# Kernel optimization log

Measured on AMD Instinct MI355X. Metric: run time of the kernel, lower is better.

Reference implementation:

```python
import jax, jax.numpy as jnp
import numpy as np

H = 32          # num query heads
KV = 8          # num kv heads
D = 64          # head_dim
WIN = 512       # sliding_window
BASE = 10000.0  # rope base


def setup_inputs() -> dict:
    key = jax.random.key(0)
    ks = jax.random.split(key, 5)
    B, S, DIM = 2, 2048, 2048
    x = jax.random.normal(ks[0], (B, S, DIM), dtype=jnp.float32)
    wq = jax.random.normal(ks[1], (H * D, DIM), dtype=jnp.float32) * 0.02
    wk = jax.random.normal(ks[2], (KV * D, DIM), dtype=jnp.float32) * 0.02
    wv = jax.random.normal(ks[3], (KV * D, DIM), dtype=jnp.float32) * 0.02
    wo = jax.random.normal(ks[4], (DIM, H * D), dtype=jnp.float32) * 0.02
    return {"x": x, "wq": wq, "wk": wk, "wv": wv, "wo": wo}


def _rope_tables(S):
    inv_freq = 1.0 / (BASE ** (jnp.arange(0, D, 2, dtype=jnp.float32) / D))
    t = jnp.arange(S, dtype=jnp.float32)
    freqs = t[:, None] * inv_freq[None, :]          # [S, D/2]
    emb = jnp.concatenate([freqs, freqs], axis=-1)  # [S, D]
    return jnp.cos(emb)[:, None, :], jnp.sin(emb)[:, None, :]  # [S,1,D]


def _rotate_half(u):
    return jnp.concatenate([-u[..., D // 2:], u[..., :D // 2]], axis=-1)


def reference(x, wq, wk, wv, wo):
    B, S, _ = x.shape
    q = (x @ wq.T).reshape(B, S, H, D)
    k = (x @ wk.T).reshape(B, S, KV, D)
    v = (x @ wv.T).reshape(B, S, KV, D)

    cos, sin = _rope_tables(S)  # [S,1,D] broadcasts over batch and heads
    q = q * cos + _rotate_half(q) * sin
    k = k * cos + _rotate_half(k) * sin

    q = q.transpose(0, 2, 1, 3)                        # [B,H,S,D]
    k = jnp.repeat(k.transpose(0, 2, 1, 3), H // KV, axis=1)  # [B,H,S,D]
    v = jnp.repeat(v.transpose(0, 2, 1, 3), H // KV, axis=1)

    scale = 1.0 / jnp.sqrt(jnp.float32(D))
    scores = jnp.einsum('bhqd,bhkd->bhqk', q, k) * scale  # [B,H,S,S]

    i = jnp.arange(S)[:, None]
    j = jnp.arange(S)[None, :]
    window_mask = jnp.abs(i - j) > WIN // 2   # True = masked (outside window)
    causal_mask = j > i                        # True = masked (future)
    masked = window_mask | causal_mask
    scores = jnp.where(masked[None, None], -jnp.inf, scores)

    attn = jax.nn.softmax(scores, axis=-1)
    out = jnp.einsum('bhqk,bhkd->bhqd', attn, v)  # [B,H,S,D]
    out = out.transpose(0, 2, 1, 3).reshape(B, S, H * D)
    return out @ wo.T
```

## Files before the change

kernel.cpp:

```cpp
#include <hip/hip_runtime.h>
#include <cstdint>
#include <cstddef>

#define SLEN 2048
#define NB 2
#define NH 32
#define NKV 8
#define HD 64
#define MROWS 4096
#define QDIM 2048
#define KVDIM 512
#define WINH 256

typedef float f32x4 __attribute__((ext_vector_type(4)));
typedef __bf16 bf16x8 __attribute__((ext_vector_type(8)));

__device__ __forceinline__ unsigned short f2bf(float f) {
  union { float f; unsigned u; } v; v.f = f;
  unsigned r = v.u + 0x7fffu + ((v.u >> 16) & 1u);
  return (unsigned short)(r >> 16);
}
__device__ __forceinline__ float bf2f(unsigned short h) {
  union { unsigned u; float f; } v; v.u = ((unsigned)h) << 16;
  return v.f;
}
__device__ __forceinline__ unsigned pk2(float a, float b) {
  return (unsigned)f2bf(a) | ((unsigned)f2bf(b) << 16);
}
__device__ __forceinline__ unsigned cvtpk(float a, float b) {
  unsigned r;
  asm("v_cvt_pk_bf16_f32 %0, %1, %2" : "=v"(r) : "v"(a), "v"(b));
  return r;
}
__device__ __forceinline__ uint4 cvt16(float4 a, float4 b) {
  uint4 u;
  u.x = pk2(a.x, a.y); u.y = pk2(a.z, a.w);
  u.z = pk2(b.x, b.y); u.w = pk2(b.z, b.w);
  return u;
}
__device__ __forceinline__ void async16(const unsigned short* g, unsigned short* l) {
  __builtin_amdgcn_global_load_lds(
      (const __attribute__((address_space(1))) unsigned int*)g,
      (__attribute__((address_space(3))) unsigned int*)l, 16, 0, 0);
}

__global__ void conv_xw(const float* __restrict__ x,
                        const float* __restrict__ wq, const float* __restrict__ wk,
                        const float* __restrict__ wv,
                        unsigned short* __restrict__ xb, unsigned short* __restrict__ wqkvb,
                        float2* __restrict__ tab) {
  size_t t = (size_t)blockIdx.x * 256 + threadIdx.x;
  if (t < (size_t)1048576) {
    size_t e = t * 8;
    float4 a = *(const float4*)(x + e);
    float4 b = *(const float4*)(x + e + 4);
    *(uint4*)(xb + e) = cvt16(a, b);
  } else if (t < (size_t)1835008) {
    size_t e = (t - 1048576) * 8;
    int row = (int)(e >> 11);
    const float* src; size_t off;
    if (row < 2048)       { src = wq; off = e; }
    else if (row < 2560)  { src = wk; off = e - (size_t)2048 * 2048; }
    else                  { src = wv; off = e - (size_t)2560 * 2048; }
    float4 a = *(const float4*)(src + off);
    float4 b = *(const float4*)(src + off + 4);
    *(uint4*)(wqkvb + e) = cvt16(a, b);
  } else {
    int id = (int)(t - 1835008);
    int d = id & 31;
    int s = id >> 5;
    float inv = expf((float)d * (-2.0f / 64.0f) * 9.210340371976184f);
    float ang = (float)s * inv;
    float sn, cs;
    sincosf(ang, &sn, &cs);
    tab[id] = make_float2(cs, sn);
  }
}

__global__ void rope_qk(unsigned short* __restrict__ qb,
                        unsigned short* __restrict__ kb,
                        const float* __restrict__ tabf) {
  const float2* tab = (const float2*)tabf;
  int tid = blockIdx.x * 256 + threadIdx.x;
  int oct = tid & 3;
  int head = (tid >> 2) % 40;
  int row = tid / 160;
  int s = row & (SLEN - 1);
  int d0 = oct * 8;
  unsigned short* p = (head < NH)
      ? qb + (size_t)row * QDIM + head * HD
      : kb + (size_t)row * KVDIM + (head - NH) * HD;
  uint4 u0 = *(const uint4*)(p + d0);
  uint4 u1 = *(const uint4*)(p + d0 + 32);
  const unsigned short* a16 = (const unsigned short*)&u0;
  const unsigned short* b16 = (const unsigned short*)&u1;
  unsigned short o0[8], o1[8];
#pragma unroll
  for (int j = 0; j < 8; ++j) {
    float2 cs = tab[s * 32 + d0 + j];
    float a = bf2f(a16[j]), b = bf2f(b16[j]);
    o0[j] = f2bf(a * cs.x - b * cs.y);
    o1[j] = f2bf(b * cs.x + a * cs.y);
  }
  *(uint4*)(p + d0)      = *(const uint4*)o0;
  *(uint4*)(p + d0 + 32) = *(const uint4*)o1;
}

__global__ __launch_bounds__(512, 2) void qkv_gemm(
    const unsigned short* __restrict__ Ap, const unsigned short* __restrict__ Bp,
    unsigned short* __restrict__ o_q, unsigned short* __restrict__ o_k,
    unsigned short* __restrict__ o_v)
{
  extern __shared__ unsigned short L[];
  constexpr int NT = 32;

  const int bid = blockIdx.x;
  const int swz = (bid & 7) * 32 + (bid >> 3);
  const int bm0 = (swz & 15) * 256;
  const int bn0 = (swz >> 4) * 192;

  const int tid = threadIdx.x;
  const int lane = tid & 63, wid = tid >> 6;
  const int g = lane >> 4, cl = lane & 15;
  const int wm = wid >> 2, wn = wid & 3;

  const int r0 = wid * 32 + (lane >> 2);
  const int s0 = (((lane & 3) ^ ((lane >> 3) & 3)) << 3);
  const unsigned short* gA = Ap + (size_t)(bm0 + r0) * 2048 + s0;
  const unsigned short* gB = Bp + (size_t)(bn0 + r0) * 2048 + s0;

  const int slotus = ((g ^ ((cl >> 1) & 3)) << 3);
  const int aread = (wm * 128 + cl) * 32 + slotus;
  const int bread = (wn * 48 + cl) * 32 + slotus;

#define REG_(b, op, kh) ((((b) * 2 + (op)) * 2 + (kh)) * 8192)
#define STG(op, kh, tt, db) do { \
    const unsigned short* s_ = ((op) ? gB : gA) + (tt) * 64 + (kh) * 32; \
    unsigned short* d_ = L + REG_(db, op, kh) + wid * 1024; \
    async16(s_, d_); \
    async16(s_ + 16 * 2048, d_ + 512); \
  } while (0)
#define LDA(dst, kh, mh) \
    _Pragma("unroll") for (int mf = 0; mf < 4; ++mf) \
      dst[mf] = *(const bf16x8*)&L[REG_(cb, 0, kh) + aread + (mh) * 2048 + mf * 512];
#define LDB(dst, kh) \
    _Pragma("unroll") for (int nf = 0; nf < 3; ++nf) \
      dst[nf] = *(const bf16x8*)&L[REG_(cb, 1, kh) + bread + nf * 512];
#define MM(mh, A, B) do { \
    __builtin_amdgcn_s_setprio(1); \
    _Pragma("unroll") for (int mf = 0; mf < 4; ++mf) \
      _Pragma("unroll") for (int nf = 0; nf < 3; ++nf) \
        acc[(mh) * 4 + mf][nf] = __builtin_amdgcn_mfma_f32_16x16x32_bf16( \
            A[mf], B[nf], acc[(mh) * 4 + mf][nf], 0, 0, 0); \
    __builtin_amdgcn_s_setprio(0); \
  } while (0)

  f32x4 acc[8][3] = {};

  STG(0, 0, 0, 0); STG(1, 0, 0, 0); STG(0, 1, 0, 0); STG(1, 1, 0, 0);
  STG(0, 0, 1, 1); STG(1, 0, 1, 1);
  asm volatile("s_waitcnt vmcnt(4)" ::: "memory");
  __builtin_amdgcn_s_barrier();
  __builtin_amdgcn_sched_barrier(0);

#pragma unroll 1
  for (int t = 0; t < NT; ++t) {
    const int cb = t & 1, nb = cb ^ 1;
    bf16x8 a00[4], a10[4], a01[4], a11[4], b0[3], b1[3];

    if (t + 1 < NT) STG(0, 1, t + 1, nb);
    LDA(a00, 0, 0); LDB(b0, 0);
    if (t + 1 < NT) STG(1, 1, t + 1, nb);
    LDA(a10, 0, 1);
    MM(0, a00, b0);
    LDA(a01, 1, 0); LDB(b1, 1);
    MM(1, a10, b0);
    asm volatile("s_waitcnt lgkmcnt(0)" ::: "memory");
    __builtin_amdgcn_s_barrier();
    __builtin_amdgcn_sched_barrier(0);
    if (t + 2 < NT) STG(0, 0, t + 2, cb);
    LDA(a11, 1, 1);
    MM(0, a01, b1);
    if (t + 2 < NT) STG(1, 0, t + 2, cb);
    MM(1, a11, b1);
    if (t + 2 < NT) { asm volatile("s_waitcnt vmcnt(4)" ::: "memory"); }
    else            { asm volatile("s_waitcnt vmcnt(0)" ::: "memory"); }
    asm volatile("s_waitcnt lgkmcnt(0)" ::: "memory");
    __builtin_amdgcn_s_barrier();
    __builtin_amdgcn_sched_barrier(0);
  }
#undef MM
#undef LDB
#undef LDA
#undef STG
#undef REG_

  const int rb = bm0 + wm * 128;
#pragma unroll
  for (int m = 0; m < 8; ++m)
#pragma unroll
    for (int nf = 0; nf < 3; ++nf) {
      const int col = bn0 + wn * 48 + nf * 16 + cl;
      if (col < QDIM) {
#pragma unroll
        for (int p = 0; p < 4; ++p) {
          int row = rb + m * 16 + g * 4 + p;
          o_q[(size_t)row * QDIM + col] = f2bf(acc[m][nf][p]);
        }
      } else if (col < QDIM + KVDIM) {
#pragma unroll
        for (int p = 0; p < 4; ++p) {
          int row = rb + m * 16 + g * 4 + p;
          o_k[(size_t)row * KVDIM + col - QDIM] = f2bf(acc[m][nf][p]);
        }
      } else {
        int vc = col - QDIM - KVDIM;
        int kvh = vc >> 6, d = vc & 63;
        int row0 = rb + m * 16 + g * 4;
        int bb = row0 >> 11, s = row0 & (SLEN - 1);
        unsigned short* dst = o_v + (((size_t)(bb * NKV + kvh) * HD + d) << 11) + s;
        uint2 u;
        u.x = pk2(acc[m][nf][0], acc[m][nf][1]);
        u.y = pk2(acc[m][nf][2], acc[m][nf][3]);
        *(uint2*)dst = u;
      }
    }
}

__global__ __launch_bounds__(512, 2) void out_gemm(
    const unsigned short* __restrict__ Ap, const unsigned short* __restrict__ Bp,
    float* __restrict__ o_f)
{
  extern __shared__ unsigned short L[];
  constexpr int NT = 32;

  const int bid = blockIdx.x;
  const int swz = (bid & 7) * 32 + (bid >> 3);
  const int bm0 = (swz & 31) * 128;
  const int bn0 = (swz >> 5) * 256;

  const int tid = threadIdx.x;
  const int lane = tid & 63, wid = tid >> 6;
  const int g = lane >> 4, cl = lane & 15;
  const int wm = wid >> 2, wn = wid & 3;

  const int s0 = (((lane & 3) ^ ((lane >> 3) & 3)) << 3);
  const unsigned short* gA = Ap + (size_t)(bm0 + wid * 16 + (lane >> 2)) * 2048 + s0;
  const unsigned short* gB = Bp + (size_t)(bn0 + wid * 32 + (lane >> 2)) * 2048 + s0;

  const int slotus = ((g ^ ((cl >> 1) & 3)) << 3);
  const int aread = (wm * 64 + cl) * 32 + slotus;
  const int bread = (wn * 64 + cl) * 32 + slotus;

#define REGA_(b, kh) ((b) * 24576 + (kh) * 4096)
#define REGB_(b, kh) ((b) * 24576 + 8192 + (kh) * 8192)
#define STGA(kh, tt, db) \
    async16(gA + (tt) * 64 + (kh) * 32, L + REGA_(db, kh) + wid * 512)
#define STGB(kh, tt, db) do { \
    const unsigned short* s_ = gB + (tt) * 64 + (kh) * 32; \
    unsigned short* d_ = L + REGB_(db, kh) + wid * 1024; \
    async16(s_, d_); \
    async16(s_ + 16 * 2048, d_ + 512); \
  } while (0)
#define LA(dst, kh, mp) \
    _Pragma("unroll") for (int mf = 0; mf < 2; ++mf) \
      dst[mf] = *(const bf16x8*)&L[REGA_(cb, kh) + aread + (mp) * 1024 + mf * 512];
#define LB(dst, kh) \
    _Pragma("unroll") for (int nf = 0; nf < 4; ++nf) \
      dst[nf] = *(const bf16x8*)&L[REGB_(cb, kh) + bread + nf * 512];
#define MMO(mp, A, B) do { \
    __builtin_amdgcn_s_setprio(1); \
    _Pragma("unroll") for (int mf = 0; mf < 2; ++mf) \
      _Pragma("unroll") for (int nf = 0; nf < 4; ++nf) \
        acc[(mp) * 2 + mf][nf] = __builtin_amdgcn_mfma_f32_16x16x32_bf16( \
            A[mf], B[nf], acc[(mp) * 2 + mf][nf], 0, 0, 0); \
    __builtin_amdgcn_s_setprio(0); \
  } while (0)

  f32x4 acc[4][4] = {};

  STGA(0, 0, 0); STGB(0, 0, 0); STGA(1, 0, 0); STGB(1, 0, 0);
  STGA(0, 1, 1); STGB(0, 1, 1);
  asm volatile("s_waitcnt vmcnt(3)" ::: "memory");
  __builtin_amdgcn_s_barrier();
  __builtin_amdgcn_sched_barrier(0);

#pragma unroll 1
  for (int t = 0; t < NT; ++t) {
    const int cb = t & 1, nb = cb ^ 1;
    bf16x8 p00[2], p10[2], p01[2], p11[2], b0[4], b1[4];

    if (t + 1 < NT) STGA(1, t + 1, nb);
    LA(p00, 0, 0); LB(b0, 0);
    if (t + 1 < NT) STGB(1, t + 1, nb);
    LA(p10, 0, 1);
    MMO(0, p00, b0);
    LA(p01, 1, 0); LB(b1, 1);
    MMO(1, p10, b0);
    asm volatile("s_waitcnt lgkmcnt(0)" ::: "memory");
    __builtin_amdgcn_s_barrier();
    __builtin_amdgcn_sched_barrier(0);
    if (t + 2 < NT) STGA(0, t + 2, cb);
    LA(p11, 1, 1);
    MMO(0, p01, b1);
    if (t + 2 < NT) STGB(0, t + 2, cb);
    MMO(1, p11, b1);
    if (t + 2 < NT) { asm volatile("s_waitcnt vmcnt(3)" ::: "memory"); }
    else            { asm volatile("s_waitcnt vmcnt(0)" ::: "memory"); }
    asm volatile("s_waitcnt lgkmcnt(0)" ::: "memory");
    __builtin_amdgcn_s_barrier();
    __builtin_amdgcn_sched_barrier(0);
  }
#undef MMO
#undef LB
#undef LA
#undef STGB
#undef STGA
#undef REGB_
#undef REGA_

  const int rb = bm0 + wm * 64;
  const int colb = bn0 + wn * 64;
#pragma unroll
  for (int m = 0; m < 4; ++m)
#pragma unroll
    for (int nf = 0; nf < 4; ++nf)
#pragma unroll
      for (int p = 0; p < 4; ++p) {
        int row = rb + m * 16 + g * 4 + p;
        o_f[(size_t)row * 2048 + colb + nf * 16 + cl] = acc[m][nf][p];
      }
}

__global__ __launch_bounds__(256) void attn(
    const unsigned short* __restrict__ qb, const unsigned short* __restrict__ kb,
    const unsigned short* __restrict__ vt, unsigned short* __restrict__ ao,
    const float* __restrict__ wo, unsigned short* __restrict__ wob)
{
  if (blockIdx.x >= 1024) {
    size_t t = (size_t)(blockIdx.x - 1024) * 256 + threadIdx.x;
    size_t e = t * 8;
    float4 a = *(const float4*)(wo + e);
    float4 b = *(const float4*)(wo + e + 4);
    *(uint4*)(wob + e) = cvt16(a, b);
    return;
  }

  __shared__ __align__(16) unsigned short Plds[4][2][16][40];
  const int lane = threadIdx.x & 63, wid = threadIdx.x >> 6;
  const int g = lane >> 4, cl = lane & 15;
  const int qt = blockIdx.x * 4 + wid;
  const int bh = qt >> 6, tl = qt & 63;
  const int i0 = tl * 32;
  const int b = bh >> 5, h = bh & 31, kvh = (bh & 31) >> 2;
  const int qi0 = i0 + cl, qi1 = i0 + 16 + cl;

  const unsigned short* qp0 = qb + ((size_t)(b * SLEN + qi0) * NH + h) * HD + g * 8;
  const unsigned short* qp1 = qb + ((size_t)(b * SLEN + qi1) * NH + h) * HD + g * 8;
  bf16x8 qf00 = *(const bf16x8*)qp0, qf01 = *(const bf16x8*)(qp0 + 32);
  bf16x8 qf10 = *(const bf16x8*)qp1, qf11 = *(const bf16x8*)(qp1 + 32);

  const unsigned short* kbase = kb + ((size_t)b * SLEN * NKV + kvh) * HD + g * 8;
  const unsigned short* vbase = vt + ((size_t)(b * NKV + kvh) * HD) * SLEN;

  f32x4 acc0[4] = {}, acc1[4] = {};
  float m0 = -1e30f, l0 = 0.f, m1 = -1e30f, l1 = 0.f;
  const int jb = (i0 > WINH) ? (i0 - WINH) : 0;

#define LOADK(dst, jj) do { \
    _Pragma("unroll") for (int t = 0; t < 2; ++t) { \
      int krow = (jj) + 16 * t + cl; \
      if (krow > SLEN - 1) krow = SLEN - 1; \
      const unsigned short* kp_ = kbase + (size_t)krow * KVDIM; \
      dst[t * 2]     = *(const bf16x8*)kp_; \
      dst[t * 2 + 1] = *(const bf16x8*)(kp_ + 32); \
    } \
  } while (0)

#define LOADV(dst, jj) do { \
    int jv = (jj) + g * 8; \
    if (jv > SLEN - 8) jv = SLEN - 8; \
    _Pragma("unroll") for (int vb2 = 0; vb2 < 4; ++vb2) \
      dst[vb2] = *(const bf16x8*)(vbase + (size_t)(vb2 * 16 + cl) * SLEN + jv); \
  } while (0)

#define SOFTMAX(SAC, MR, LR, ACC, QI, QF) do { \
    float sm[2][4]; float mx = -1e30f; \
    _Pragma("unroll") for (int t = 0; t < 2; ++t) \
      _Pragma("unroll") for (int p = 0; p < 4; ++p) { \
        int kj = j0 + 16 * t + 4 * g + p; \
        bool ok = (kj <= (QI)) && ((QI) - kj <= WINH); \
        float v = ok ? SAC[t][p] * 0.125f : -1e30f; \
        sm[t][p] = v; mx = fmaxf(mx, v); \
      } \
    mx = fmaxf(mx, __shfl_xor(mx, 16)); \
    mx = fmaxf(mx, __shfl_xor(mx, 32)); \
    float mnew = fmaxf(MR, mx); \
    float corr = __expf(MR - mnew); \
    float ps = 0.f; unsigned pw00, pw01, pw10, pw11; \
    { \
      float p0 = __expf(sm[0][0] - mnew), p1 = __expf(sm[0][1] - mnew); \
      float p2 = __expf(sm[0][2] - mnew), p3 = __expf(sm[0][3] - mnew); \
      ps += p0 + p1 + p2 + p3; pw00 = cvtpk(p0, p1); pw01 = cvtpk(p2, p3); \
      float p4 = __expf(sm[1][0] - mnew), p5 = __expf(sm[1][1] - mnew); \
      float p6 = __expf(sm[1][2] - mnew), p7 = __expf(sm[1][3] - mnew); \
      ps += p4 + p5 + p6 + p7; pw10 = cvtpk(p4, p5); pw11 = cvtpk(p6, p7); \
    } \
    ps += __shfl_xor(ps, 16); ps += __shfl_xor(ps, 32); \
    LR = LR * corr + ps; MR = mnew; \
    _Pragma("unroll") for (int vb2 = 0; vb2 < 4; ++vb2) \
      _Pragma("unroll") for (int p = 0; p < 4; ++p) ACC[vb2][p] *= corr; \
    *(unsigned*)&Plds[wid][QF][cl][4 * g]          = pw00; \
    *(unsigned*)&Plds[wid][QF][cl][4 * g + 2]      = pw01; \
    *(unsigned*)&Plds[wid][QF][cl][16 + 4 * g]     = pw10; \
    *(unsigned*)&Plds[wid][QF][cl][16 + 4 * g + 2] = pw11; \
  } while (0)

#define BODY(KC, KN, VC, VN) do { \
    LOADK(KN, j0 + 32);                           \
    LOADV(VN, j0 + 32);                           \
    f32x4 s0[2], s1[2]; \
    _Pragma("unroll") for (int t = 0; t < 2; ++t) { \
      f32x4 z = {}; \
      z = __builtin_amdgcn_mfma_f32_16x16x32_bf16(KC[t * 2], qf00, z, 0, 0, 0); \
      z = __builtin_amdgcn_mfma_f32_16x16x32_bf16(KC[t * 2 + 1], qf01, z, 0, 0, 0); \
      s0[t] = z; \
      f32x4 z2 = {}; \
      z2 = __builtin_amdgcn_mfma_f32_16x16x32_bf16(KC[t * 2], qf10, z2, 0, 0, 0); \
      z2 = __builtin_amdgcn_mfma_f32_16x16x32_bf16(KC[t * 2 + 1], qf11, z2, 0, 0, 0); \
      s1[t] = z2; \
    } \
    SOFTMAX(s0, m0, l0, acc0, qi0, 0); \
    SOFTMAX(s1, m1, l1, acc1, qi1, 1); \
    bf16x8 pf0 = *(const bf16x8*)&Plds[wid][0][cl][g * 8]; \
    bf16x8 pf1 = *(const bf16x8*)&Plds[wid][1][cl][g * 8]; \
    _Pragma("unroll") for (int vb2 = 0; vb2 < 4; ++vb2) \
      acc0[vb2] = __builtin_amdgcn_mfma_f32_16x16x32_bf16(VC[vb2], pf0, acc0[vb2], 0, 0, 0); \
    _Pragma("unroll") for (int vb2 = 0; vb2 < 4; ++vb2) \
      acc1[vb2] = __builtin_amdgcn_mfma_f32_16x16x32_bf16(VC[vb2], pf1, acc1[vb2], 0, 0, 0); \
  } while (0)

  bf16x8 kA[4], kB[4], vA[4], vB[4];
  LOADK(kA, jb); LOADV(vA, jb);
  int j0 = jb;
  for (;;) {
    BODY(kA, kB, vA, vB); j0 += 32; if (j0 > i0) break;
    BODY(kB, kA, vB, vA); j0 += 32; if (j0 > i0) break;
  }
#undef BODY
#undef SOFTMAX
#undef LOADV
#undef LOADK

  float inv0 = 1.0f / l0, inv1 = 1.0f / l1;
  unsigned short* op0 = ao + ((size_t)(b * SLEN + qi0) * NH + h) * HD;
  unsigned short* op1 = ao + ((size_t)(b * SLEN + qi1) * NH + h) * HD;
#pragma unroll
  for (int vbk = 0; vbk < 4; ++vbk) {
    *(unsigned*)(op0 + vbk * 16 + g * 4)     = cvtpk(acc0[vbk][0] * inv0, acc0[vbk][1] * inv0);
    *(unsigned*)(op0 + vbk * 16 + g * 4 + 2) = cvtpk(acc0[vbk][2] * inv0, acc0[vbk][3] * inv0);
    *(unsigned*)(op1 + vbk * 16 + g * 4)     = cvtpk(acc1[vbk][0] * inv1, acc1[vbk][1] * inv1);
    *(unsigned*)(op1 + vbk * 16 + g * 4 + 2) = cvtpk(acc1[vbk][2] * inv1, acc1[vbk][3] * inv1);
  }
}

extern "C" void kernel_launch(void* const* d_in, const int* in_sizes, int n_in,
                              void* d_out, int out_size, void* d_ws, size_t ws_size,
                              hipStream_t stream) {
  const float* x  = (const float*)d_in[0];
  const float* wq = (const float*)d_in[1];
  const float* wk = (const float*)d_in[2];
  const float* wv = (const float*)d_in[3];
  const float* wo = (const float*)d_in[4];
  float* out = (float*)d_out;

  char* w = (char*)d_ws;
  unsigned short* wqkvb = (unsigned short*)w; w += (size_t)3136 * 2048 * 2;
  unsigned short* xb    = (unsigned short*)w; w += (size_t)MROWS * QDIM * 2;
  unsigned short* qb    = (unsigned short*)w; w += (size_t)MROWS * QDIM * 2;
  unsigned short* kb    = (unsigned short*)w; w += (size_t)MROWS * KVDIM * 2;
  unsigned short* vt    = (unsigned short*)w; w += (size_t)MROWS * KVDIM * 2;
  float* tab            = (float*)w;          w += (size_t)SLEN * 32 * 8;
  unsigned short* wob = wqkvb;
  unsigned short* ao  = xb;

  hipFuncSetAttribute((const void*)qkv_gemm,
                      hipFuncAttributeMaxDynamicSharedMemorySize, 131072);
  hipFuncSetAttribute((const void*)out_gemm,
                      hipFuncAttributeMaxDynamicSharedMemorySize, 98304);

  conv_xw<<<7424, 256, 0, stream>>>(x, wq, wk, wv, xb, wqkvb, (float2*)tab);
  qkv_gemm<<<256, 512, 131072, stream>>>(xb, wqkvb, qb, kb, vt);
  rope_qk<<<(MROWS * 40 * 4) / 256, 256, 0, stream>>>(qb, kb, tab);
  attn<<<3072, 256, 0, stream>>>(qb, kb, vt, ao, wo, wob);
  out_gemm<<<256, 512, 98304, stream>>>(ao, wob, out);
}
```

Baseline: 158.6 us.

## Simplify QKV GEMM to K=32 double-buffered steps with halved LDS

The QKV projection GEMM now walks K in 64 steps of 32 rather than 32 steps of 64. It uses a plain double buffer and drops the interleaved two-half prefetch pipeline that ran two tiles ahead. Dynamic shared memory falls from 128KB to 64KB, which may let more blocks share a CU. The cost is twice as many barriers, and each step ends with a full vmcnt(0) wait, so global loads overlap less with MFMA work.

```diff
diff --git a/kernel.cpp b/kernel.cpp
--- a/kernel.cpp
+++ b/kernel.cpp
@@ -112,7 +112,7 @@
     unsigned short* __restrict__ o_v)
 {
   extern __shared__ unsigned short L[];
-  constexpr int NT = 32;
+  constexpr int NT = 64;
 
   const int bid = blockIdx.x;
   const int swz = (bid & 7) * 32 + (bid >> 3);
@@ -133,67 +133,48 @@
   const int aread = (wm * 128 + cl) * 32 + slotus;
   const int bread = (wn * 48 + cl) * 32 + slotus;
 
-#define REG_(b, op, kh) ((((b) * 2 + (op)) * 2 + (kh)) * 8192)
-#define STG(op, kh, tt, db) do { \
-    const unsigned short* s_ = ((op) ? gB : gA) + (tt) * 64 + (kh) * 32; \
-    unsigned short* d_ = L + REG_(db, op, kh) + wid * 1024; \
+#define STG32(op, tt, db) do { \
+    const unsigned short* s_ = ((op) ? gB : gA) + (tt) * 32; \
+    unsigned short* d_ = L + (db) * 16384 + (op) * 8192 + wid * 1024; \
     async16(s_, d_); \
     async16(s_ + 16 * 2048, d_ + 512); \
   } while (0)
-#define LDA(dst, kh, mh) \
-    _Pragma("unroll") for (int mf = 0; mf < 4; ++mf) \
-      dst[mf] = *(const bf16x8*)&L[REG_(cb, 0, kh) + aread + (mh) * 2048 + mf * 512];
-#define LDB(dst, kh) \
-    _Pragma("unroll") for (int nf = 0; nf < 3; ++nf) \
-      dst[nf] = *(const bf16x8*)&L[REG_(cb, 1, kh) + bread + nf * 512];
-#define MM(mh, A, B) do { \
-    __builtin_amdgcn_s_setprio(1); \
-    _Pragma("unroll") for (int mf = 0; mf < 4; ++mf) \
-      _Pragma("unroll") for (int nf = 0; nf < 3; ++nf) \
-        acc[(mh) * 4 + mf][nf] = __builtin_amdgcn_mfma_f32_16x16x32_bf16( \
-            A[mf], B[nf], acc[(mh) * 4 + mf][nf], 0, 0, 0); \
-    __builtin_amdgcn_s_setprio(0); \
-  } while (0)
 
   f32x4 acc[8][3] = {};
 
-  STG(0, 0, 0, 0); STG(1, 0, 0, 0); STG(0, 1, 0, 0); STG(1, 1, 0, 0);
-  STG(0, 0, 1, 1); STG(1, 0, 1, 1);
-  asm volatile("s_waitcnt vmcnt(4)" ::: "memory");
+  STG32(0, 0, 0); STG32(1, 0, 0);
+  asm volatile("s_waitcnt vmcnt(0)" ::: "memory");
   __builtin_amdgcn_s_barrier();
   __builtin_amdgcn_sched_barrier(0);
 
 #pragma unroll 1
   for (int t = 0; t < NT; ++t) {
     const int cb = t & 1, nb = cb ^ 1;
-    bf16x8 a00[4], a10[4], a01[4], a11[4], b0[3], b1[3];
-
-    if (t + 1 < NT) STG(0, 1, t + 1, nb);
-    LDA(a00, 0, 0); LDB(b0, 0);
-    if (t + 1 < NT) STG(1, 1, t + 1, nb);
-    LDA(a10, 0, 1);
-    MM(0, a00, b0);
-    LDA(a01, 1, 0); LDB(b1, 1);
-    MM(1, a10, b0);
+    if (t + 1 < NT) { STG32(0, t + 1, nb); STG32(1, t + 1, nb); }
+
+    bf16x8 af[8], bv[3];
+#pragma unroll
+    for (int mf = 0; mf < 8; ++mf)
+      af[mf] = *(const bf16x8*)&L[cb * 16384 + aread + mf * 512];
+#pragma unroll
+    for (int nf = 0; nf < 3; ++nf)
+      bv[nf] = *(const bf16x8*)&L[cb * 16384 + 8192 + bread + nf * 512];
+
+    __builtin_amdgcn_s_setprio(1);
+#pragma unroll
+    for (int mf = 0; mf < 8; ++mf)
+#pragma unroll
+      for (int nf = 0; nf < 3; ++nf)
+        acc[mf][nf] = __builtin_amdgcn_mfma_f32_16x16x32_bf16(
+            af[mf], bv[nf], acc[mf][nf], 0, 0, 0);
+    __builtin_amdgcn_s_setprio(0);
+
+    asm volatile("s_waitcnt vmcnt(0)" ::: "memory");
     asm volatile("s_waitcnt lgkmcnt(0)" ::: "memory");
     __builtin_amdgcn_s_barrier();
     __builtin_amdgcn_sched_barrier(0);
-    if (t + 2 < NT) STG(0, 0, t + 2, cb);
-    LDA(a11, 1, 1);
-    MM(0, a01, b1);
-    if (t + 2 < NT) STG(1, 0, t + 2, cb);
-    MM(1, a11, b1);
-    if (t + 2 < NT) { asm volatile("s_waitcnt vmcnt(4)" ::: "memory"); }
-    else            { asm volatile("s_waitcnt vmcnt(0)" ::: "memory"); }
-    asm volatile("s_waitcnt lgkmcnt(0)" ::: "memory");
-    __builtin_amdgcn_s_barrier();
-    __builtin_amdgcn_sched_barrier(0);
-  }
-#undef MM
-#undef LDB
-#undef LDA
-#undef STG
-#undef REG_
+  }
+#undef STG32
 
   const int rb = bm0 + wm * 128;
 #pragma unroll
@@ -485,12 +466,12 @@
   unsigned short* ao  = xb;
 
   hipFuncSetAttribute((const void*)qkv_gemm,
-                      hipFuncAttributeMaxDynamicSharedMemorySize, 131072);
+                      hipFuncAttributeMaxDynamicSharedMemorySize, 65536);
   hipFuncSetAttribute((const void*)out_gemm,
                       hipFuncAttributeMaxDynamicSharedMemorySize, 98304);
 
   conv_xw<<<7424, 256, 0, stream>>>(x, wq, wk, wv, xb, wqkvb, (float2*)tab);
-  qkv_gemm<<<256, 512, 131072, stream>>>(xb, wqkvb, qb, kb, vt);
+  qkv_gemm<<<256, 512, 65536, stream>>>(xb, wqkvb, qb, kb, vt);
   rope_qk<<<(MROWS * 40 * 4) / 256, 256, 0, stream>>>(qb, kb, tab);
   attn<<<3072, 256, 0, stream>>>(qb, kb, vt, ao, wo, wob);
   out_gemm<<<256, 512, 98304, stream>>>(ao, wob, out);
```

Result: slower. 166.8 us (+5.2%).
